# Kernel optimization log

Measured on AMD Instinct MI355X. Metric: run time of the kernel, lower is better.

Reference implementation:

```python
import jax, jax.numpy as jnp
import numpy as np

B, S, D = 4, 2048, 1024

def setup_inputs() -> dict:
    key = jax.random.key(0)
    kx, kq, kk, kv = jax.random.split(key, 4)
    glorot = (6.0 / (D + D)) ** 0.5
    return {
        "x": jax.random.normal(kx, (B, S, D), dtype=jnp.float32),
        "Wq": jax.random.uniform(kq, (D, D), jnp.float32, -glorot, glorot),
        "Wk": jax.random.uniform(kk, (D, D), jnp.float32, -glorot, glorot),
        "Wv": jax.random.uniform(kv, (D, D), jnp.float32, -glorot, glorot),
    }

def reference(x, Wq, Wk, Wv):
    # q,k,v: [B,S,D]
    q = jnp.einsum("bsd,de->bse", x, Wq)
    k = jnp.einsum("bsd,de->bse", x, Wk)
    v = jnp.einsum("bsd,de->bse", x, Wv)
    scale = jnp.sqrt(jnp.asarray(q.shape[-1], q.dtype))
    scores = jnp.einsum("bqd,bkd->bqk", q, k) / scale  # [B,S,S]
    w = jax.nn.softmax(scores, axis=-1)
    return jnp.einsum("bqk,bkd->bqd", w, v)
```

## Files before the change

### kernel.cpp

```cpp
#include <hip/hip_runtime.h>
#include <hip/hip_bf16.h>


typedef _Float16 half_t;
typedef _Float16 half8 __attribute__((ext_vector_type(8)));
typedef _Float16 half4v __attribute__((ext_vector_type(4)));
typedef float f32x4 __attribute__((ext_vector_type(4)));

__device__ __forceinline__ void load16_to_lds(const half_t* g, half_t* l) {
  __builtin_amdgcn_global_load_lds(
      (const __attribute__((address_space(1))) void*)g,
      (__attribute__((address_space(3))) void*)l, 16, 0, 0);
}

#define LGKM0 asm volatile("s_waitcnt lgkmcnt(0)" ::: "memory")
#define LGKM8 asm volatile("s_waitcnt lgkmcnt(8)" ::: "memory")
#define VM0   asm volatile("s_waitcnt vmcnt(0)" ::: "memory")
#define VM4   asm volatile("s_waitcnt vmcnt(4)" ::: "memory")
#define VM6   asm volatile("s_waitcnt vmcnt(6)" ::: "memory")
#define BAR   __builtin_amdgcn_s_barrier()
#define PRIO1 __builtin_amdgcn_s_setprio(1)
#define PRIO0 __builtin_amdgcn_s_setprio(0)

__global__ __launch_bounds__(512, 2) void qkvt_gemm8(
    const half_t* __restrict__ xh, const half_t* __restrict__ wt,
    half_t* __restrict__ qk, half_t* __restrict__ vtg) {
  __shared__ __align__(16) half_t As[2][256 * 64];
  __shared__ __align__(16) half_t Bs[2][256 * 64];

  const int b = blockIdx.x;
  const int x = b & 7, j = b >> 3;
  const int m0 = (x * 4 + (j & 3)) * 256;
  const int n0 = (j >> 2) * 256;

  const int t     = threadIdx.x;
  const int lane  = t & 63;
  const int wave  = t >> 6;
  const int wr128 = (wave >> 2) * 128;
  const int wc64  = (wave & 3) * 64;
  const int lm    = lane & 15;
  const int lq    = lane >> 4;
  const int pos0  = (lq ^ (lm & 7)) * 8;
  const int pos1  = ((4 + lq) ^ (lm & 7)) * 8;
  const int t8    = t * 8;

  const int trow = t >> 3;
  const int tchk = (t & 7) ^ (trow & 7);
  const half_t* gA0 = xh + (size_t)(m0 + trow) * 1024 + tchk * 8;
  const half_t* gB0 = wt + (size_t)(n0 + trow) * 1024 + tchk * 8;

  f32x4 acc[8][4] = {};
  half8 va[4][2], vb0[2][2], vb1[2][2];

#define ST_A(buf, h, kt) do {                                                  \
    load16_to_lds(gA0 + (size_t)((h)*128) * 1024 + (size_t)(kt) * 64,          \
                  &As[buf][(h)*128*64] + t8);                                  \
    load16_to_lds(gA0 + (size_t)((h)*128+64) * 1024 + (size_t)(kt) * 64,       \
                  &As[buf][((h)*128+64)*64] + t8);                             \
  } while (0)
#define ST_B(buf, h, kt) do {                                                  \
    load16_to_lds(gB0 + (size_t)((h)*128) * 1024 + (size_t)(kt) * 64,          \
                  &Bs[buf][(h)*128*64] + t8);                                  \
    load16_to_lds(gB0 + (size_t)((h)*128+64) * 1024 + (size_t)(kt) * 64,       \
                  &Bs[buf][((h)*128+64)*64] + t8);                             \
  } while (0)
#define RD_A(buf, mh) do {                                                     \
    _Pragma("unroll") for (int m = 0; m < 4; ++m) {                            \
      const int ar = wr128 + (mh)*64 + m * 16 + lm;                            \
      va[m][0] = *(const half8*)&As[buf][ar * 64 + pos0];                      \
      va[m][1] = *(const half8*)&As[buf][ar * 64 + pos1];                      \
    } } while (0)
#define RD_B(buf, nh, vb) do {                                                 \
    _Pragma("unroll") for (int n = 0; n < 2; ++n) {                            \
      const int br = wc64 + (nh)*32 + n * 16 + lm;                             \
      vb[n][0] = *(const half8*)&Bs[buf][br * 64 + pos0];                      \
      vb[n][1] = *(const half8*)&Bs[buf][br * 64 + pos1];                      \
    } } while (0)
#define MF_Q(mh, nh, vb) do {                                                  \
    _Pragma("unroll") for (int kk = 0; kk < 2; ++kk)                           \
    _Pragma("unroll") for (int m = 0; m < 4; ++m)                              \
    _Pragma("unroll") for (int n = 0; n < 2; ++n)                              \
      acc[(mh)*4+m][(nh)*2+n] = __builtin_amdgcn_mfma_f32_16x16x32_f16(        \
          va[m][kk], vb[n][kk], acc[(mh)*4+m][(nh)*2+n], 0, 0, 0);             \
  } while (0)

  ST_A(0, 0, 0); ST_A(0, 1, 0);
  ST_B(0, 0, 0); ST_B(0, 1, 0);
  ST_B(1, 0, 1); ST_B(1, 1, 1);
  VM4;
  BAR;

#pragma unroll 1
  for (int i = 0; i < 8; ++i) {
    const int st1 = (2 * i + 1 < 15) ? 2 * i + 1 : 15;
    const int st2 = (2 * i + 2 < 15) ? 2 * i + 2 : 15;
    const int st3 = (2 * i + 3 < 15) ? 2 * i + 3 : 15;
    RD_A(0, 0); RD_B(0, 0, vb0);
    ST_A(1, 0, st1);
    LGKM8;
    BAR; LGKM0;
    PRIO1; MF_Q(0, 0, vb0); PRIO0;
    BAR;
    RD_B(0, 1, vb1);
    ST_A(1, 1, st1);
    BAR; LGKM0;
    PRIO1; MF_Q(0, 1, vb1); PRIO0;
    BAR;
    RD_A(0, 1);
    ST_B(0, 0, st2);
    BAR; LGKM0;
    PRIO1; MF_Q(1, 0, vb0); PRIO0;
    BAR;
    ST_B(0, 1, st2);
    BAR; LGKM0;
    PRIO1; MF_Q(1, 1, vb1); PRIO0;
    VM4;
    BAR;
    RD_A(1, 0); RD_B(1, 0, vb0);
    ST_A(0, 0, st2);
    LGKM8;
    BAR; LGKM0;
    PRIO1; MF_Q(0, 0, vb0); PRIO0;
    BAR;
    RD_B(1, 1, vb1);
    ST_A(0, 1, st2);
    BAR; LGKM0;
    PRIO1; MF_Q(0, 1, vb1); PRIO0;
    BAR;
    RD_A(1, 1);
    ST_B(1, 0, st3);
    BAR; LGKM0;
    PRIO1; MF_Q(1, 0, vb0); PRIO0;
    BAR;
    ST_B(1, 1, st3);
    BAR; LGKM0;
    PRIO1; MF_Q(1, 1, vb1); PRIO0;
    VM4;
    BAR;
  }

#pragma unroll
  for (int m = 0; m < 8; ++m)
#pragma unroll
    for (int n = 0; n < 4; ++n) {
      const int col = n0 + wc64 + n * 16 + lm;
#pragma unroll
      for (int r = 0; r < 4; ++r) {
        const int row = m0 + wr128 + m * 16 + lq * 4 + r;
        qk[(size_t)row * 2048 + col] = (half_t)acc[m][n][r];
      }
    }
#undef ST_A
#undef ST_B
#undef RD_A
#undef RD_B
#undef MF_Q

  const int m0v = (j >> 2) * 128;
  const int n0v = (x * 4 + (j & 3)) * 256;
  const int wmv = (wave >> 2) * 64;
  const int wnv = (wave & 3) * 64;

  const half_t* gA2 = wt + (size_t)2 * 1024 * 1024 +
                      (size_t)(m0v + trow) * 1024 + tchk * 8;
  const half_t* gB2 = xh + (size_t)(n0v + trow) * 1024 + tchk * 8;

  f32x4 acc2[4][4] = {};

#define ST_A2(buf, kt) do {                                                    \
    load16_to_lds(gA2 + (size_t)(kt) * 64, &As[buf][0] + t8);                  \
    load16_to_lds(gA2 + (size_t)64 * 1024 + (size_t)(kt) * 64,                 \
                  &As[buf][64*64] + t8);                                       \
  } while (0)
#define ST_B2(buf, h, kt) do {                                                 \
    load16_to_lds(gB2 + (size_t)((h)*128) * 1024 + (size_t)(kt) * 64,          \
                  &Bs[buf][(h)*128*64] + t8);                                  \
    load16_to_lds(gB2 + (size_t)((h)*128+64) * 1024 + (size_t)(kt) * 64,       \
                  &Bs[buf][((h)*128+64)*64] + t8);                             \
  } while (0)
#define RD_A2(buf, mh) do {                                                    \
    _Pragma("unroll") for (int m = 0; m < 2; ++m) {                            \
      const int ar = wmv + (mh)*32 + m * 16 + lm;                              \
      va[(mh)*2+m][0] = *(const half8*)&As[buf][ar * 64 + pos0];               \
      va[(mh)*2+m][1] = *(const half8*)&As[buf][ar * 64 + pos1];               \
    } } while (0)
#define RD_B2(buf, nh, vb) do {                                                \
    _Pragma("unroll") for (int n = 0; n < 2; ++n) {                            \
      const int br = wnv + (nh)*32 + n * 16 + lm;                              \
      vb[n][0] = *(const half8*)&Bs[buf][br * 64 + pos0];                      \
      vb[n][1] = *(const half8*)&Bs[buf][br * 64 + pos1];                      \
    } } while (0)
#define MF_V(mh, nh, vb) do {                                                  \
    _Pragma("unroll") for (int kk = 0; kk < 2; ++kk)                           \
    _Pragma("unroll") for (int m = 0; m < 2; ++m)                              \
    _Pragma("unroll") for (int n = 0; n < 2; ++n)                              \
      acc2[(mh)*2+m][(nh)*2+n] = __builtin_amdgcn_mfma_f32_16x16x32_f16(       \
          va[(mh)*2+m][kk], vb[n][kk], acc2[(mh)*2+m][(nh)*2+n], 0, 0, 0);     \
  } while (0)

  VM0;
  ST_B2(0, 0, 0); ST_B2(0, 1, 0); ST_A2(0, 0);
  ST_B2(1, 0, 1); ST_B2(1, 1, 1); ST_A2(1, 1);
  VM6;
  BAR;

#pragma unroll 1
  for (int i = 0; i < 8; ++i) {
    const int t2 = (2 * i + 2 < 15) ? 2 * i + 2 : 15;
    const int t3 = (2 * i + 3 < 15) ? 2 * i + 3 : 15;
    RD_A2(0, 0); RD_B2(0, 0, vb0);
    BAR; LGKM0;
    PRIO1; MF_V(0, 0, vb0); PRIO0;
    BAR;
    RD_B2(0, 1, vb1);
    BAR; LGKM0;
    PRIO1; MF_V(0, 1, vb1); PRIO0;
    BAR;
    RD_A2(0, 1);
    ST_B2(0, 0, t2);
    BAR; LGKM0;
    PRIO1; MF_V(1, 0, vb0); PRIO0;
    BAR;
    ST_B2(0, 1, t2); ST_A2(0, t2);
    BAR; LGKM0;
    PRIO1; MF_V(1, 1, vb1); PRIO0;
    VM6;
    BAR;
    RD_A2(1, 0); RD_B2(1, 0, vb0);
    BAR; LGKM0;
    PRIO1; MF_V(0, 0, vb0); PRIO0;
    BAR;
    RD_B2(1, 1, vb1);
    BAR; LGKM0;
    PRIO1; MF_V(0, 1, vb1); PRIO0;
    BAR;
    RD_A2(1, 1);
    ST_B2(1, 0, t3);
    BAR; LGKM0;
    PRIO1; MF_V(1, 0, vb0); PRIO0;
    BAR;
    ST_B2(1, 1, t3); ST_A2(1, t3);
    BAR; LGKM0;
    PRIO1; MF_V(1, 1, vb1); PRIO0;
    VM6;
    BAR;
  }

#pragma unroll
  for (int m = 0; m < 4; ++m)
#pragma unroll
    for (int n = 0; n < 4; ++n) {
      const int col = n0v + wnv + n * 16 + lm;
#pragma unroll
      for (int r = 0; r < 4; ++r) {
        const int row = m0v + wmv + m * 16 + lq * 4 + r;
        vtg[(size_t)row * 8192 + col] = (half_t)acc2[m][n][r];
      }
    }
#undef ST_A2
#undef ST_B2
#undef RD_A2
#undef RD_B2
#undef MF_V
}

__global__ __launch_bounds__(512, 2) void scores_gemm8(
    const half_t* __restrict__ qk, half_t* __restrict__ sc,
    float* __restrict__ lpart) {
  __shared__ __align__(16) half_t As[2][256 * 64];
  __shared__ __align__(16) half_t Bs[2][256 * 64];

  const int id  = blockIdx.x;
  const int x   = id & 7, j = id >> 3;
  const int bx  = j & 7;
  const int z   = x >> 1;
  const int by  = (x & 1) * 4 + (j >> 3);
  const int m0  = by * 256;
  const int n0  = bx * 256;
  const half_t* A  = qk + (size_t)z * 2048 * 2048;
  const half_t* Bm = A + 1024;
  half_t* C = sc + (size_t)z * 2048 * 2048;

  const int t     = threadIdx.x;
  const int lane  = t & 63;
  const int wave  = t >> 6;
  const int wr128 = (wave >> 2) * 128;
  const int wc64  = (wave & 3) * 64;
  const int lm    = lane & 15;
  const int lq    = lane >> 4;
  const int pos0  = (lq ^ (lm & 7)) * 8;
  const int pos1  = ((4 + lq) ^ (lm & 7)) * 8;
  const int t8    = t * 8;

  const int trow = t >> 3;
  const int tchk = (t & 7) ^ (trow & 7);
  const half_t* gA0 = A  + (size_t)(m0 + trow) * 2048 + tchk * 8;
  const half_t* gB0 = Bm + (size_t)(n0 + trow) * 2048 + tchk * 8;

  f32x4 acc[8][4] = {};
  half8 va[4][2], vb0[2][2], vb1[2][2];

#define ST_A(buf, h, kt) do {                                                  \
    load16_to_lds(gA0 + (size_t)((h)*128) * 2048 + (size_t)(kt) * 64,          \
                  &As[buf][(h)*128*64] + t8);                                  \
    load16_to_lds(gA0 + (size_t)((h)*128+64) * 2048 + (size_t)(kt) * 64,       \
                  &As[buf][((h)*128+64)*64] + t8);                             \
  } while (0)
#define ST_B(buf, h, kt) do {                                                  \
    load16_to_lds(gB0 + (size_t)((h)*128) * 2048 + (size_t)(kt) * 64,          \
                  &Bs[buf][(h)*128*64] + t8);                                  \
    load16_to_lds(gB0 + (size_t)((h)*128+64) * 2048 + (size_t)(kt) * 64,       \
                  &Bs[buf][((h)*128+64)*64] + t8);                             \
  } while (0)
#define RD_A(buf, mh) do {                                                     \
    _Pragma("unroll") for (int m = 0; m < 4; ++m) {                            \
      const int ar = wr128 + (mh)*64 + m * 16 + lm;                            \
      va[m][0] = *(const half8*)&As[buf][ar * 64 + pos0];                      \
      va[m][1] = *(const half8*)&As[buf][ar * 64 + pos1];                      \
    } } while (0)
#define RD_B(buf, nh, vb) do {                                                 \
    _Pragma("unroll") for (int n = 0; n < 2; ++n) {                            \
      const int br = wc64 + (nh)*32 + n * 16 + lm;                             \
      vb[n][0] = *(const half8*)&Bs[buf][br * 64 + pos0];                      \
      vb[n][1] = *(const half8*)&Bs[buf][br * 64 + pos1];                      \
    } } while (0)
#define MF_Q(mh, nh, vb) do {                                                  \
    _Pragma("unroll") for (int kk = 0; kk < 2; ++kk)                           \
    _Pragma("unroll") for (int m = 0; m < 4; ++m)                              \
    _Pragma("unroll") for (int n = 0; n < 2; ++n)                              \
      acc[(mh)*4+m][(nh)*2+n] = __builtin_amdgcn_mfma_f32_16x16x32_f16(        \
          va[m][kk], vb[n][kk], acc[(mh)*4+m][(nh)*2+n], 0, 0, 0);             \
  } while (0)

  ST_A(0, 0, 0); ST_A(0, 1, 0);
  ST_B(0, 0, 0); ST_B(0, 1, 0);
  ST_B(1, 0, 1); ST_B(1, 1, 1);
  VM4;
  BAR;

#pragma unroll 1
  for (int i = 0; i < 8; ++i) {
    const int st1 = (2 * i + 1 < 15) ? 2 * i + 1 : 15;
    const int st2 = (2 * i + 2 < 15) ? 2 * i + 2 : 15;
    const int st3 = (2 * i + 3 < 15) ? 2 * i + 3 : 15;
    RD_A(0, 0); RD_B(0, 0, vb0);
    ST_A(1, 0, st1);
    LGKM8;
    BAR; LGKM0;
    PRIO1; MF_Q(0, 0, vb0); PRIO0;
    BAR;
    RD_B(0, 1, vb1);
    ST_A(1, 1, st1);
    BAR; LGKM0;
    PRIO1; MF_Q(0, 1, vb1); PRIO0;
    BAR;
    RD_A(0, 1);
    ST_B(0, 0, st2);
    BAR; LGKM0;
    PRIO1; MF_Q(1, 0, vb0); PRIO0;
    BAR;
    ST_B(0, 1, st2);
    BAR; LGKM0;
    PRIO1; MF_Q(1, 1, vb1); PRIO0;
    VM4;
    BAR;
    RD_A(1, 0); RD_B(1, 0, vb0);
    ST_A(0, 0, st2);
    LGKM8;
    BAR; LGKM0;
    PRIO1; MF_Q(0, 0, vb0); PRIO0;
    BAR;
    RD_B(1, 1, vb1);
    ST_A(0, 1, st2);
    BAR; LGKM0;
    PRIO1; MF_Q(0, 1, vb1); PRIO0;
    BAR;
    RD_A(1, 1);
    ST_B(1, 0, st3);
    BAR; LGKM0;
    PRIO1; MF_Q(1, 0, vb0); PRIO0;
    BAR;
    ST_B(1, 1, st3);
    BAR; LGKM0;
    PRIO1; MF_Q(1, 1, vb1); PRIO0;
    VM4;
    BAR;
  }

  const float scale = 1.0f / 32.0f;
#pragma unroll
  for (int m = 0; m < 8; ++m)
#pragma unroll
    for (int r = 0; r < 4; ++r) {
      const int row = m0 + wr128 + m * 16 + lq * 4 + r;
      float s = 0.f;
#pragma unroll
      for (int n = 0; n < 4; ++n) {
        const int col = n0 + wc64 + n * 16 + lm;
        float v = __expf(acc[m][n][r] * scale - 8.0f);
        s += v;
        C[(size_t)row * 2048 + col] = (half_t)v;
      }
      s += __shfl_xor(s, 1); s += __shfl_xor(s, 2);
      s += __shfl_xor(s, 4); s += __shfl_xor(s, 8);
      if (lm == 0)
        lpart[((size_t)z * 2048 + row) * 32 + bx * 4 + (wave & 3)] = s;
    }
#undef ST_A
#undef ST_B
#undef RD_A
#undef RD_B
#undef MF_Q
}

__global__ __launch_bounds__(512, 2) void pv_gemm8(
    const half_t* __restrict__ sc, const half_t* __restrict__ vtg,
    float* __restrict__ out, const float* __restrict__ lpart) {
  __shared__ __align__(16) half_t As[2][128 * 64];
  __shared__ __align__(16) half_t Bs[2][256 * 64];
  __shared__ float linv[128];

  const int id = blockIdx.x;
  const int x  = id & 7, j = id >> 3;
  const int z  = x >> 1;
  const int m0 = ((x & 1) * 8 + (j >> 2)) * 128;
  const int n0 = (j & 3) * 256;
  const half_t* A  = sc  + (size_t)z * 2048 * 2048;
  const half_t* Bm = vtg + (size_t)z * 2048;
  float* C = out + (size_t)z * 2048 * 1024;

  const int t    = threadIdx.x;
  const int lane = t & 63;
  const int wave = t >> 6;
  const int wmv  = (wave >> 2) * 64;
  const int wnv  = (wave & 3) * 64;
  const int lm   = lane & 15;
  const int lq   = lane >> 4;
  const int pos0 = (lq ^ (lm & 7)) * 8;
  const int pos1 = ((4 + lq) ^ (lm & 7)) * 8;
  const int t8   = t * 8;

  if (t < 128) {
    const float4* lp = (const float4*)&lpart[((size_t)z * 2048 + m0 + t) * 32];
    float s = 0.f;
#pragma unroll
    for (int p = 0; p < 8; ++p) {
      float4 v = lp[p];
      s += v.x + v.y + v.z + v.w;
    }
    linv[t] = 1.0f / s;
  }

  const int trow = t >> 3;
  const int tchk = (t & 7) ^ (trow & 7);
  const half_t* gA2 = A  + (size_t)(m0 + trow) * 2048 + tchk * 8;
  const half_t* gB2 = Bm + (size_t)(n0 + trow) * 8192 + tchk * 8;

  f32x4 acc2[4][4] = {};
  half8 va[4][2], vb0[2][2], vb1[2][2];

#define ST_A2(buf, kt) do {                                                    \
    load16_to_lds(gA2 + (size_t)(kt) * 64, &As[buf][0] + t8);                  \
    load16_to_lds(gA2 + (size_t)64 * 2048 + (size_t)(kt) * 64,                 \
                  &As[buf][64*64] + t8);                                       \
  } while (0)
#define ST_B2(buf, h, kt) do {                                                 \
    load16_to_lds(gB2 + (size_t)((h)*128) * 8192 + (size_t)(kt) * 64,          \
                  &Bs[buf][(h)*128*64] + t8);                                  \
    load16_to_lds(gB2 + (size_t)((h)*128+64) * 8192 + (size_t)(kt) * 64,       \
                  &Bs[buf][((h)*128+64)*64] + t8);                             \
  } while (0)
#define RD_A2(buf, mh) do {                                                    \
    _Pragma("unroll") for (int m = 0; m < 2; ++m) {                            \
      const int ar = wmv + (mh)*32 + m * 16 + lm;                              \
      va[(mh)*2+m][0] = *(const half8*)&As[buf][ar * 64 + pos0];               \
      va[(mh)*2+m][1] = *(const half8*)&As[buf][ar * 64 + pos1];               \
    } } while (0)
#define RD_B2(buf, nh, vb) do {                                                \
    _Pragma("unroll") for (int n = 0; n < 2; ++n) {                            \
      const int br = wnv + (nh)*32 + n * 16 + lm;                              \
      vb[n][0] = *(const half8*)&Bs[buf][br * 64 + pos0];                      \
      vb[n][1] = *(const half8*)&Bs[buf][br * 64 + pos1];                      \
    } } while (0)
#define MF_V(mh, nh, vb) do {                                                  \
    _Pragma("unroll") for (int kk = 0; kk < 2; ++kk)                           \
    _Pragma("unroll") for (int m = 0; m < 2; ++m)                              \
    _Pragma("unroll") for (int n = 0; n < 2; ++n)                              \
      acc2[(mh)*2+m][(nh)*2+n] = __builtin_amdgcn_mfma_f32_16x16x32_f16(       \
          va[(mh)*2+m][kk], vb[n][kk], acc2[(mh)*2+m][(nh)*2+n], 0, 0, 0);     \
  } while (0)

  ST_B2(0, 0, 0); ST_B2(0, 1, 0); ST_A2(0, 0);
  ST_B2(1, 0, 1); ST_B2(1, 1, 1); ST_A2(1, 1);
  VM6;
  BAR;

#pragma unroll 1
  for (int i = 0; i < 16; ++i) {
    const int t2 = (2 * i + 2 < 31) ? 2 * i + 2 : 31;
    const int t3 = (2 * i + 3 < 31) ? 2 * i + 3 : 31;
    RD_A2(0, 0); RD_B2(0, 0, vb0);
    BAR; LGKM0;
    PRIO1; MF_V(0, 0, vb0); PRIO0;
    BAR;
    RD_B2(0, 1, vb1);
    BAR; LGKM0;
    PRIO1; MF_V(0, 1, vb1); PRIO0;
    BAR;
    RD_A2(0, 1);
    ST_B2(0, 0, t2);
    BAR; LGKM0;
    PRIO1; MF_V(1, 0, vb0); PRIO0;
    BAR;
    ST_B2(0, 1, t2); ST_A2(0, t2);
    BAR; LGKM0;
    PRIO1; MF_V(1, 1, vb1); PRIO0;
    VM6;
    BAR;
    RD_A2(1, 0); RD_B2(1, 0, vb0);
    BAR; LGKM0;
    PRIO1; MF_V(0, 0, vb0); PRIO0;
    BAR;
    RD_B2(1, 1, vb1);
    BAR; LGKM0;
    PRIO1; MF_V(0, 1, vb1); PRIO0;
    BAR;
    RD_A2(1, 1);
    ST_B2(1, 0, t3);
    BAR; LGKM0;
    PRIO1; MF_V(1, 0, vb0); PRIO0;
    BAR;
    ST_B2(1, 1, t3); ST_A2(1, t3);
    BAR; LGKM0;
    PRIO1; MF_V(1, 1, vb1); PRIO0;
    VM6;
    BAR;
  }

#pragma unroll
  for (int m = 0; m < 4; ++m)
#pragma unroll
    for (int r = 0; r < 4; ++r) {
      const int lrow = wmv + m * 16 + lq * 4 + r;
      const float inv = linv[lrow];
      const int row = m0 + lrow;
#pragma unroll
      for (int n = 0; n < 4; ++n) {
        const int col = n0 + wnv + n * 16 + lm;
        C[(size_t)row * 1024 + col] = acc2[m][n][r] * inv;
      }
    }
#undef ST_A2
#undef ST_B2
#undef RD_A2
#undef RD_B2
#undef MF_V
}

__global__ __launch_bounds__(256) void prep(
    const float* __restrict__ x, half_t* __restrict__ xh,
    const float* __restrict__ Wq, const float* __restrict__ Wk,
    const float* __restrict__ Wv, half_t* __restrict__ wt) {
  __shared__ half_t tile[32][33];
  const int b = blockIdx.x;
  const int t = threadIdx.x;
  if (b < 8192) {
    const int i = (b * 256 + t) * 4;
    const float4 v = *reinterpret_cast<const float4*>(x + i);
    half4v o;
    o.x = (half_t)v.x; o.y = (half_t)v.y; o.z = (half_t)v.z; o.w = (half_t)v.w;
    *reinterpret_cast<half4v*>(xh + i) = o;
  } else {
    int bb = b - 8192;
    const int w = bb >> 10; bb &= 1023;
    const float* in = (w == 0) ? Wq : (w == 1) ? Wk : Wv;
    half_t* o = wt + (size_t)w * 1024 * 1024;
    const int r0 = (bb >> 5) * 32, c0 = (bb & 31) * 32;
    const int tx = t & 31, ty = t >> 5;
#pragma unroll
    for (int i = 0; i < 32; i += 8)
      tile[ty + i][tx] = (half_t)in[(size_t)(r0 + ty + i) * 1024 + c0 + tx];
    __syncthreads();
#pragma unroll
    for (int i = 0; i < 32; i += 8)
      o[(size_t)(c0 + ty + i) * 1024 + r0 + tx] = tile[tx][ty + i];
  }
}

extern "C" void kernel_launch(void* const* d_in, const int* in_sizes, int n_in,
                              void* d_out, int out_size, void* d_ws, size_t ws_size,
                              hipStream_t stream) {
  constexpr int Bb = 4, S = 2048, D = 1024;
  constexpr size_t MS = (size_t)Bb * S;

  const float* x  = (const float*)d_in[0];
  const float* Wq = (const float*)d_in[1];
  const float* Wk = (const float*)d_in[2];
  const float* Wv = (const float*)d_in[3];
  float* out = (float*)d_out;

  char* p = (char*)d_ws;
  half_t* xh    = (half_t*)p; p += MS * D * 2;
  half_t* wt    = (half_t*)p; p += (size_t)3 * D * D * 2;
  half_t* qk    = (half_t*)p; p += MS * (size_t)(2 * D) * 2;
  half_t* vtg   = (half_t*)p; p += (size_t)D * MS * 2;
  half_t* sc    = (half_t*)p; p += (size_t)Bb * S * S * 2;
  float*  lpart = (float*)p;  p += MS * 32 * 4;

  prep<<<11264, 256, 0, stream>>>(x, xh, Wq, Wk, Wv, wt);
  qkvt_gemm8<<<256, 512, 0, stream>>>(xh, wt, qk, vtg);
  scores_gemm8<<<256, 512, 0, stream>>>(qk, sc, lpart);
  pv_gemm8<<<256, 512, 0, stream>>>(sc, vtg, out, lpart);
}
```

Before: 220.7 us.

## Fuse prep and three GEMM kernels into one cooperative persistent kernel

Merges the fp16 conversion/transpose prep kernel, the QKV projection GEMM, the scores GEMM and the PV GEMM into a single cooperative kernel of 256 blocks, with grid-wide syncs between phases. The prep work is redistributed across the 256 blocks, and the weight-transpose tiles reuse the GEMM's shared-memory buffers. This removes three kernel launches and their inter-kernel gaps. In exchange it adds grid-barrier cost and ties the grid size to full co-residency. It also enlarges the shared footprint, because the PV phase now shares 256-row A buffers.

```diff
diff --git a/kernel.cpp b/kernel.cpp
--- a/kernel.cpp
+++ b/kernel.cpp
@@ -1,5 +1,8 @@
 #include <hip/hip_runtime.h>
 #include <hip/hip_bf16.h>
+#include <hip/hip_cooperative_groups.h>
+
+namespace cg = cooperative_groups;
 
 
 typedef _Float16 half_t;
@@ -22,35 +25,78 @@
 #define PRIO1 __builtin_amdgcn_s_setprio(1)
 #define PRIO0 __builtin_amdgcn_s_setprio(0)
 
-__global__ __launch_bounds__(512, 2) void qkvt_gemm8(
-    const half_t* __restrict__ xh, const half_t* __restrict__ wt,
-    half_t* __restrict__ qk, half_t* __restrict__ vtg) {
+__global__ __launch_bounds__(512, 2) void fused_attn(
+    const float* __restrict__ x, const float* __restrict__ Wq,
+    const float* __restrict__ Wk, const float* __restrict__ Wv,
+    half_t* __restrict__ xh, half_t* __restrict__ wt,
+    half_t* __restrict__ qk, half_t* __restrict__ vtg,
+    half_t* __restrict__ sc, float* __restrict__ lpart,
+    float* __restrict__ out) {
   __shared__ __align__(16) half_t As[2][256 * 64];
   __shared__ __align__(16) half_t Bs[2][256 * 64];
-
-  const int b = blockIdx.x;
-  const int x = b & 7, j = b >> 3;
-  const int m0 = (x * 4 + (j & 3)) * 256;
-  const int n0 = (j >> 2) * 256;
-
-  const int t     = threadIdx.x;
-  const int lane  = t & 63;
-  const int wave  = t >> 6;
+  __shared__ float linv[128];
+
+  cg::grid_group gg = cg::this_grid();
+
+  const int t    = threadIdx.x;
+  const int lane = t & 63;
+  const int wave = t >> 6;
+  const int lm   = lane & 15;
+  const int lq   = lane >> 4;
+  const int pos0 = (lq ^ (lm & 7)) * 8;
+  const int pos1 = ((4 + lq) ^ (lm & 7)) * 8;
+  const int t8   = t * 8;
+  const int trow = t >> 3;
+  const int tchk = (t & 7) ^ (trow & 7);
   const int wr128 = (wave >> 2) * 128;
   const int wc64  = (wave & 3) * 64;
-  const int lm    = lane & 15;
-  const int lq    = lane >> 4;
-  const int pos0  = (lq ^ (lm & 7)) * 8;
-  const int pos1  = ((4 + lq) ^ (lm & 7)) * 8;
-  const int t8    = t * 8;
-
-  const int trow = t >> 3;
-  const int tchk = (t & 7) ^ (trow & 7);
-  const half_t* gA0 = xh + (size_t)(m0 + trow) * 1024 + tchk * 8;
-  const half_t* gB0 = wt + (size_t)(n0 + trow) * 1024 + tchk * 8;
-
-  f32x4 acc[8][4] = {};
-  half8 va[4][2], vb0[2][2], vb1[2][2];
+
+  {
+    const int gtid = blockIdx.x * 512 + t;
+#pragma unroll
+    for (int k = 0; k < 16; ++k) {
+      const size_t i = ((size_t)gtid + (size_t)k * 131072) * 4;
+      const float4 v = *reinterpret_cast<const float4*>(x + i);
+      half4v o;
+      o.x = (half_t)v.x; o.y = (half_t)v.y; o.z = (half_t)v.z; o.w = (half_t)v.w;
+      *reinterpret_cast<half4v*>(xh + i) = o;
+    }
+    half_t (*tp)[32][33] = reinterpret_cast<half_t (*)[32][33]>(&As[0][0]);
+    const int sub = t >> 8;
+    const int tt  = t & 255;
+    const int tx = tt & 31, ty = tt >> 5;
+    for (int it = 0; it < 6; ++it) {
+      const int tile = blockIdx.x * 12 + it * 2 + sub;
+      const int w    = tile >> 10;
+      const int rem  = tile & 1023;
+      const float* in = (w == 0) ? Wq : (w == 1) ? Wk : Wv;
+      half_t* o = wt + (size_t)w * 1024 * 1024;
+      const int r0 = (rem >> 5) * 32, c0 = (rem & 31) * 32;
+      __syncthreads();
+#pragma unroll
+      for (int i2 = 0; i2 < 32; i2 += 8)
+        tp[sub][ty + i2][tx] =
+            (half_t)in[(size_t)(r0 + ty + i2) * 1024 + c0 + tx];
+      __syncthreads();
+#pragma unroll
+      for (int i2 = 0; i2 < 32; i2 += 8)
+        o[(size_t)(c0 + ty + i2) * 1024 + r0 + tx] = tp[sub][tx][ty + i2];
+    }
+    VM0;
+  }
+  gg.sync();
+
+  {
+    const int b = blockIdx.x;
+    const int xc = b & 7, j = b >> 3;
+    const int m0 = (xc * 4 + (j & 3)) * 256;
+    const int n0 = (j >> 2) * 256;
+
+    const half_t* gA0 = xh + (size_t)(m0 + trow) * 1024 + tchk * 8;
+    const half_t* gB0 = wt + (size_t)(n0 + trow) * 1024 + tchk * 8;
+
+    f32x4 acc[8][4] = {};
+    half8 va[4][2], vb0[2][2], vb1[2][2];
 
 #define ST_A(buf, h, kt) do {                                                  \
     load16_to_lds(gA0 + (size_t)((h)*128) * 1024 + (size_t)(kt) * 64,          \
@@ -84,88 +130,88 @@
           va[m][kk], vb[n][kk], acc[(mh)*4+m][(nh)*2+n], 0, 0, 0);             \
   } while (0)
 
-  ST_A(0, 0, 0); ST_A(0, 1, 0);
-  ST_B(0, 0, 0); ST_B(0, 1, 0);
-  ST_B(1, 0, 1); ST_B(1, 1, 1);
-  VM4;
-  BAR;
-
-#pragma unroll 1
-  for (int i = 0; i < 8; ++i) {
-    const int st1 = (2 * i + 1 < 15) ? 2 * i + 1 : 15;
-    const int st2 = (2 * i + 2 < 15) ? 2 * i + 2 : 15;
-    const int st3 = (2 * i + 3 < 15) ? 2 * i + 3 : 15;
-    RD_A(0, 0); RD_B(0, 0, vb0);
-    ST_A(1, 0, st1);
-    LGKM8;
-    BAR; LGKM0;
-    PRIO1; MF_Q(0, 0, vb0); PRIO0;
-    BAR;
-    RD_B(0, 1, vb1);
-    ST_A(1, 1, st1);
-    BAR; LGKM0;
-    PRIO1; MF_Q(0, 1, vb1); PRIO0;
-    BAR;
-    RD_A(0, 1);
-    ST_B(0, 0, st2);
-    BAR; LGKM0;
-    PRIO1; MF_Q(1, 0, vb0); PRIO0;
-    BAR;
-    ST_B(0, 1, st2);
-    BAR; LGKM0;
-    PRIO1; MF_Q(1, 1, vb1); PRIO0;
+    ST_A(0, 0, 0); ST_A(0, 1, 0);
+    ST_B(0, 0, 0); ST_B(0, 1, 0);
+    ST_B(1, 0, 1); ST_B(1, 1, 1);
     VM4;
     BAR;
-    RD_A(1, 0); RD_B(1, 0, vb0);
-    ST_A(0, 0, st2);
-    LGKM8;
-    BAR; LGKM0;
-    PRIO1; MF_Q(0, 0, vb0); PRIO0;
-    BAR;
-    RD_B(1, 1, vb1);
-    ST_A(0, 1, st2);
-    BAR; LGKM0;
-    PRIO1; MF_Q(0, 1, vb1); PRIO0;
-    BAR;
-    RD_A(1, 1);
-    ST_B(1, 0, st3);
-    BAR; LGKM0;
-    PRIO1; MF_Q(1, 0, vb0); PRIO0;
-    BAR;
-    ST_B(1, 1, st3);
-    BAR; LGKM0;
-    PRIO1; MF_Q(1, 1, vb1); PRIO0;
-    VM4;
-    BAR;
-  }
-
-#pragma unroll
-  for (int m = 0; m < 8; ++m)
-#pragma unroll
-    for (int n = 0; n < 4; ++n) {
-      const int col = n0 + wc64 + n * 16 + lm;
-#pragma unroll
-      for (int r = 0; r < 4; ++r) {
-        const int row = m0 + wr128 + m * 16 + lq * 4 + r;
-        qk[(size_t)row * 2048 + col] = (half_t)acc[m][n][r];
+
+#pragma unroll 1
+    for (int i = 0; i < 8; ++i) {
+      const int st1 = (2 * i + 1 < 15) ? 2 * i + 1 : 15;
+      const int st2 = (2 * i + 2 < 15) ? 2 * i + 2 : 15;
+      const int st3 = (2 * i + 3 < 15) ? 2 * i + 3 : 15;
+      RD_A(0, 0); RD_B(0, 0, vb0);
+      ST_A(1, 0, st1);
+      LGKM8;
+      BAR; LGKM0;
+      PRIO1; MF_Q(0, 0, vb0); PRIO0;
+      BAR;
+      RD_B(0, 1, vb1);
+      ST_A(1, 1, st1);
+      BAR; LGKM0;
+      PRIO1; MF_Q(0, 1, vb1); PRIO0;
+      BAR;
+      RD_A(0, 1);
+      ST_B(0, 0, st2);
+      BAR; LGKM0;
+      PRIO1; MF_Q(1, 0, vb0); PRIO0;
+      BAR;
+      ST_B(0, 1, st2);
+      BAR; LGKM0;
+      PRIO1; MF_Q(1, 1, vb1); PRIO0;
+      VM4;
+      BAR;
+      RD_A(1, 0); RD_B(1, 0, vb0);
+      ST_A(0, 0, st2);
+      LGKM8;
+      BAR; LGKM0;
+      PRIO1; MF_Q(0, 0, vb0); PRIO0;
+      BAR;
+      RD_B(1, 1, vb1);
+      ST_A(0, 1, st2);
+      BAR; LGKM0;
+      PRIO1; MF_Q(0, 1, vb1); PRIO0;
+      BAR;
+      RD_A(1, 1);
+      ST_B(1, 0, st3);
+      BAR; LGKM0;
+      PRIO1; MF_Q(1, 0, vb0); PRIO0;
+      BAR;
+      ST_B(1, 1, st3);
+      BAR; LGKM0;
+      PRIO1; MF_Q(1, 1, vb1); PRIO0;
+      VM4;
+      BAR;
+    }
+
+#pragma unroll
+    for (int m = 0; m < 8; ++m)
+#pragma unroll
+      for (int n = 0; n < 4; ++n) {
+        const int col = n0 + wc64 + n * 16 + lm;
+#pragma unroll
+        for (int r = 0; r < 4; ++r) {
+          const int row = m0 + wr128 + m * 16 + lq * 4 + r;
+          qk[(size_t)row * 2048 + col] = (half_t)acc[m][n][r];
+        }
       }
-    }
 #undef ST_A
 #undef ST_B
 #undef RD_A
 #undef RD_B
 #undef MF_Q
 
-  const int m0v = (j >> 2) * 128;
-  const int n0v = (x * 4 + (j & 3)) * 256;
-  const int wmv = (wave >> 2) * 64;
-  const int wnv = (wave & 3) * 64;
-
-  const half_t* gA2 = wt + (size_t)2 * 1024 * 1024 +
-                      (size_t)(m0v + trow) * 1024 + tchk * 8;
-  const half_t* gB2 = xh + (size_t)(n0v + trow) * 1024 + tchk * 8;
-
-  f32x4 acc2[4][4] = {};
+    const int m0v = (j >> 2) * 128;
+    const int n0v = (xc * 4 + (j & 3)) * 256;
+    const int wmv = (wave >> 2) * 64;
+    const int wnv = (wave & 3) * 64;
+
+    const half_t* gA2 = wt + (size_t)2 * 1024 * 1024 +
+                        (size_t)(m0v + trow) * 1024 + tchk * 8;
+    const half_t* gB2 = xh + (size_t)(n0v + trow) * 1024 + tchk * 8;
+
+    f32x4 acc2[4][4] = {};
 
 #define ST_A2(buf, kt) do {                                                    \
     load16_to_lds(gA2 + (size_t)(kt) * 64, &As[buf][0] + t8);                  \
@@ -198,107 +244,91 @@
           va[(mh)*2+m][kk], vb[n][kk], acc2[(mh)*2+m][(nh)*2+n], 0, 0, 0);     \
   } while (0)
 
-  VM0;
-  ST_B2(0, 0, 0); ST_B2(0, 1, 0); ST_A2(0, 0);
-  ST_B2(1, 0, 1); ST_B2(1, 1, 1); ST_A2(1, 1);
-  VM6;
-  BAR;
-
-#pragma unroll 1
-  for (int i = 0; i < 8; ++i) {
-    const int t2 = (2 * i + 2 < 15) ? 2 * i + 2 : 15;
-    const int t3 = (2 * i + 3 < 15) ? 2 * i + 3 : 15;
-    RD_A2(0, 0); RD_B2(0, 0, vb0);
-    BAR; LGKM0;
-    PRIO1; MF_V(0, 0, vb0); PRIO0;
-    BAR;
-    RD_B2(0, 1, vb1);
-    BAR; LGKM0;
-    PRIO1; MF_V(0, 1, vb1); PRIO0;
-    BAR;
-    RD_A2(0, 1);
-    ST_B2(0, 0, t2);
-    BAR; LGKM0;
-    PRIO1; MF_V(1, 0, vb0); PRIO0;
-    BAR;
-    ST_B2(0, 1, t2); ST_A2(0, t2);
-    BAR; LGKM0;
-    PRIO1; MF_V(1, 1, vb1); PRIO0;
+    VM0;
+    ST_B2(0, 0, 0); ST_B2(0, 1, 0); ST_A2(0, 0);
+    ST_B2(1, 0, 1); ST_B2(1, 1, 1); ST_A2(1, 1);
     VM6;
     BAR;
-    RD_A2(1, 0); RD_B2(1, 0, vb0);
-    BAR; LGKM0;
-    PRIO1; MF_V(0, 0, vb0); PRIO0;
-    BAR;
-    RD_B2(1, 1, vb1);
-    BAR; LGKM0;
-    PRIO1; MF_V(0, 1, vb1); PRIO0;
-    BAR;
-    RD_A2(1, 1);
-    ST_B2(1, 0, t3);
-    BAR; LGKM0;
-    PRIO1; MF_V(1, 0, vb0); PRIO0;
-    BAR;
-    ST_B2(1, 1, t3); ST_A2(1, t3);
-    BAR; LGKM0;
-    PRIO1; MF_V(1, 1, vb1); PRIO0;
-    VM6;
-    BAR;
-  }
-
-#pragma unroll
-  for (int m = 0; m < 4; ++m)
-#pragma unroll
-    for (int n = 0; n < 4; ++n) {
-      const int col = n0v + wnv + n * 16 + lm;
-#pragma unroll
-      for (int r = 0; r < 4; ++r) {
-        const int row = m0v + wmv + m * 16 + lq * 4 + r;
-        vtg[(size_t)row * 8192 + col] = (half_t)acc2[m][n][r];
+
+#pragma unroll 1
+    for (int i = 0; i < 8; ++i) {
+      const int t2 = (2 * i + 2 < 15) ? 2 * i + 2 : 15;
+      const int t3 = (2 * i + 3 < 15) ? 2 * i + 3 : 15;
+      RD_A2(0, 0); RD_B2(0, 0, vb0);
+      BAR; LGKM0;
+      PRIO1; MF_V(0, 0, vb0); PRIO0;
+      BAR;
+      RD_B2(0, 1, vb1);
+      BAR; LGKM0;
+      PRIO1; MF_V(0, 1, vb1); PRIO0;
+      BAR;
+      RD_A2(0, 1);
+      ST_B2(0, 0, t2);
+      BAR; LGKM0;
+      PRIO1; MF_V(1, 0, vb0); PRIO0;
+      BAR;
+      ST_B2(0, 1, t2); ST_A2(0, t2);
+      BAR; LGKM0;
+      PRIO1; MF_V(1, 1, vb1); PRIO0;
+      VM6;
+      BAR;
+      RD_A2(1, 0); RD_B2(1, 0, vb0);
+      BAR; LGKM0;
+      PRIO1; MF_V(0, 0, vb0); PRIO0;
+      BAR;
+      RD_B2(1, 1, vb1);
+      BAR; LGKM0;
+      PRIO1; MF_V(0, 1, vb1); PRIO0;
+      BAR;
+      RD_A2(1, 1);
+      ST_B2(1, 0, t3);
+      BAR; LGKM0;
+      PRIO1; MF_V(1, 0, vb0); PRIO0;
+      BAR;
+      ST_B2(1, 1, t3); ST_A2(1, t3);
+      BAR; LGKM0;
+      PRIO1; MF_V(1, 1, vb1); PRIO0;
+      VM6;
+      BAR;
+    }
+
+#pragma unroll
+    for (int m = 0; m < 4; ++m)
+#pragma unroll
+      for (int n = 0; n < 4; ++n) {
+        const int col = n0v + wnv + n * 16 + lm;
+#pragma unroll
+        for (int r = 0; r < 4; ++r) {
+          const int row = m0v + wmv + m * 16 + lq * 4 + r;
+          vtg[(size_t)row * 8192 + col] = (half_t)acc2[m][n][r];
+        }
       }
-    }
 #undef ST_A2
 #undef ST_B2
 #undef RD_A2
 #undef RD_B2
 #undef MF_V
-}
-
-__global__ __launch_bounds__(512, 2) void scores_gemm8(
-    const half_t* __restrict__ qk, half_t* __restrict__ sc,
-    float* __restrict__ lpart) {
-  __shared__ __align__(16) half_t As[2][256 * 64];
-  __shared__ __align__(16) half_t Bs[2][256 * 64];
-
-  const int id  = blockIdx.x;
-  const int x   = id & 7, j = id >> 3;
-  const int bx  = j & 7;
-  const int z   = x >> 1;
-  const int by  = (x & 1) * 4 + (j >> 3);
-  const int m0  = by * 256;
-  const int n0  = bx * 256;
-  const half_t* A  = qk + (size_t)z * 2048 * 2048;
-  const half_t* Bm = A + 1024;
-  half_t* C = sc + (size_t)z * 2048 * 2048;
-
-  const int t     = threadIdx.x;
-  const int lane  = t & 63;
-  const int wave  = t >> 6;
-  const int wr128 = (wave >> 2) * 128;
-  const int wc64  = (wave & 3) * 64;
-  const int lm    = lane & 15;
-  const int lq    = lane >> 4;
-  const int pos0  = (lq ^ (lm & 7)) * 8;
-  const int pos1  = ((4 + lq) ^ (lm & 7)) * 8;
-  const int t8    = t * 8;
-
-  const int trow = t >> 3;
-  const int tchk = (t & 7) ^ (trow & 7);
-  const half_t* gA0 = A  + (size_t)(m0 + trow) * 2048 + tchk * 8;
-  const half_t* gB0 = Bm + (size_t)(n0 + trow) * 2048 + tchk * 8;
-
-  f32x4 acc[8][4] = {};
-  half8 va[4][2], vb0[2][2], vb1[2][2];
+    VM0;
+  }
+  gg.sync();
+
+  {
+    const int id = blockIdx.x;
+    const int xc = id & 7, j = id >> 3;
+    const int bx = j & 7;
+    const int z  = xc >> 1;
+    const int by = (xc & 1) * 4 + (j >> 3);
+    const int m0 = by * 256;
+    const int n0 = bx * 256;
+    const half_t* A  = qk + (size_t)z * 2048 * 2048;
+    const half_t* Bm = A + 1024;
+    half_t* C = sc + (size_t)z * 2048 * 2048;
+
+    const half_t* gA0 = A  + (size_t)(m0 + trow) * 2048 + tchk * 8;
+    const half_t* gB0 = Bm + (size_t)(n0 + trow) * 2048 + tchk * 8;
+
+    f32x4 acc[8][4] = {};
+    half8 va[4][2], vb0[2][2], vb1[2][2];
 
 #define ST_A(buf, h, kt) do {                                                  \
     load16_to_lds(gA0 + (size_t)((h)*128) * 2048 + (size_t)(kt) * 64,          \
@@ -332,132 +362,119 @@
           va[m][kk], vb[n][kk], acc[(mh)*4+m][(nh)*2+n], 0, 0, 0);             \
   } while (0)
 
-  ST_A(0, 0, 0); ST_A(0, 1, 0);
-  ST_B(0, 0, 0); ST_B(0, 1, 0);
-  ST_B(1, 0, 1); ST_B(1, 1, 1);
-  VM4;
-  BAR;
-
-#pragma unroll 1
-  for (int i = 0; i < 8; ++i) {
-    const int st1 = (2 * i + 1 < 15) ? 2 * i + 1 : 15;
-    const int st2 = (2 * i + 2 < 15) ? 2 * i + 2 : 15;
-    const int st3 = (2 * i + 3 < 15) ? 2 * i + 3 : 15;
-    RD_A(0, 0); RD_B(0, 0, vb0);
-    ST_A(1, 0, st1);
-    LGKM8;
-    BAR; LGKM0;
-    PRIO1; MF_Q(0, 0, vb0); PRIO0;
-    BAR;
-    RD_B(0, 1, vb1);
-    ST_A(1, 1, st1);
-    BAR; LGKM0;
-    PRIO1; MF_Q(0, 1, vb1); PRIO0;
-    BAR;
-    RD_A(0, 1);
-    ST_B(0, 0, st2);
-    BAR; LGKM0;
-    PRIO1; MF_Q(1, 0, vb0); PRIO0;
-    BAR;
-    ST_B(0, 1, st2);
-    BAR; LGKM0;
-    PRIO1; MF_Q(1, 1, vb1); PRIO0;
+    ST_A(0, 0, 0); ST_A(0, 1, 0);
+    ST_B(0, 0, 0); ST_B(0, 1, 0);
+    ST_B(1, 0, 1); ST_B(1, 1, 1);
     VM4;
     BAR;
-    RD_A(1, 0); RD_B(1, 0, vb0);
-    ST_A(0, 0, st2);
-    LGKM8;
-    BAR; LGKM0;
-    PRIO1; MF_Q(0, 0, vb0); PRIO0;
-    BAR;
-    RD_B(1, 1, vb1);
-    ST_A(0, 1, st2);
-    BAR; LGKM0;
-    PRIO1; MF_Q(0, 1, vb1); PRIO0;
-    BAR;
-    RD_A(1, 1);
-    ST_B(1, 0, st3);
-    BAR; LGKM0;
-    PRIO1; MF_Q(1, 0, vb0); PRIO0;
-    BAR;
-    ST_B(1, 1, st3);
-    BAR; LGKM0;
-    PRIO1; MF_Q(1, 1, vb1); PRIO0;
-    VM4;
-    BAR;
-  }
-
-  const float scale = 1.0f / 32.0f;
-#pragma unroll
-  for (int m = 0; m < 8; ++m)
-#pragma unroll
-    for (int r = 0; r < 4; ++r) {
-      const int row = m0 + wr128 + m * 16 + lq * 4 + r;
-      float s = 0.f;
-#pragma unroll
-      for (int n = 0; n < 4; ++n) {
-        const int col = n0 + wc64 + n * 16 + lm;
-        float v = __expf(acc[m][n][r] * scale - 8.0f);
-        s += v;
-        C[(size_t)row * 2048 + col] = (half_t)v;
+
+#pragma unroll 1
+    for (int i = 0; i < 8; ++i) {
+      const int st1 = (2 * i + 1 < 15) ? 2 * i + 1 : 15;
+      const int st2 = (2 * i + 2 < 15) ? 2 * i + 2 : 15;
+      const int st3 = (2 * i + 3 < 15) ? 2 * i + 3 : 15;
+      RD_A(0, 0); RD_B(0, 0, vb0);
+      ST_A(1, 0, st1);
+      LGKM8;
+      BAR; LGKM0;
+      PRIO1; MF_Q(0, 0, vb0); PRIO0;
+      BAR;
+      RD_B(0, 1, vb1);
+      ST_A(1, 1, st1);
+      BAR; LGKM0;
+      PRIO1; MF_Q(0, 1, vb1); PRIO0;
+      BAR;
+      RD_A(0, 1);
+      ST_B(0, 0, st2);
+      BAR; LGKM0;
+      PRIO1; MF_Q(1, 0, vb0); PRIO0;
+      BAR;
+      ST_B(0, 1, st2);
+      BAR; LGKM0;
+      PRIO1; MF_Q(1, 1, vb1); PRIO0;
+      VM4;
+      BAR;
+      RD_A(1, 0); RD_B(1, 0, vb0);
+      ST_A(0, 0, st2);
+      LGKM8;
+      BAR; LGKM0;
+      PRIO1; MF_Q(0, 0, vb0); PRIO0;
+      BAR;
+      RD_B(1, 1, vb1);
+      ST_A(0, 1, st2);
+      BAR; LGKM0;
+      PRIO1; MF_Q(0, 1, vb1); PRIO0;
+      BAR;
+      RD_A(1, 1);
+      ST_B(1, 0, st3);
+      BAR; LGKM0;
+      PRIO1; MF_Q(1, 0, vb0); PRIO0;
+      BAR;
+      ST_B(1, 1, st3);
+      BAR; LGKM0;
+      PRIO1; MF_Q(1, 1, vb1); PRIO0;
+      VM4;
+      BAR;
+    }
+
+    const float scale = 1.0f / 32.0f;
+#pragma unroll
+    for (int m = 0; m < 8; ++m)
+#pragma unroll
+      for (int r = 0; r < 4; ++r) {
+        const int row = m0 + wr128 + m * 16 + lq * 4 + r;
+        float s = 0.f;
+#pragma unroll
+        for (int n = 0; n < 4; ++n) {
+          const int col = n0 + wc64 + n * 16 + lm;
+          float v = __expf(acc[m][n][r] * scale - 8.0f);
+          s += v;
+          C[(size_t)row * 2048 + col] = (half_t)v;
+        }
+        s += __shfl_xor(s, 1); s += __shfl_xor(s, 2);
+        s += __shfl_xor(s, 4); s += __shfl_xor(s, 8);
+        if (lm == 0)
+          lpart[((size_t)z * 2048 + row) * 32 + bx * 4 + (wave & 3)] = s;
       }
-      s += __shfl_xor(s, 1); s += __shfl_xor(s, 2);
-      s += __shfl_xor(s, 4); s += __shfl_xor(s, 8);
-      if (lm == 0)
-        lpart[((size_t)z * 2048 + row) * 32 + bx * 4 + (wave & 3)] = s;
-    }
 #undef ST_A
 #undef ST_B
 #undef RD_A
 #undef RD_B
 #undef MF_Q
-}
-
-__global__ __launch_bounds__(512, 2) void pv_gemm8(
-    const half_t* __restrict__ sc, const half_t* __restrict__ vtg,
-    float* __restrict__ out, const float* __restrict__ lpart) {
-  __shared__ __align__(16) half_t As[2][128 * 64];
-  __shared__ __align__(16) half_t Bs[2][256 * 64];
-  __shared__ float linv[128];
-
-  const int id = blockIdx.x;
-  const int x  = id & 7, j = id >> 3;
-  const int z  = x >> 1;
-  const int m0 = ((x & 1) * 8 + (j >> 2)) * 128;
-  const int n0 = (j & 3) * 256;
-  const half_t* A  = sc  + (size_t)z * 2048 * 2048;
-  const half_t* Bm = vtg + (size_t)z * 2048;
-  float* C = out + (size_t)z * 2048 * 1024;
-
-  const int t    = threadIdx.x;
-  const int lane = t & 63;
-  const int wave = t >> 6;
-  const int wmv  = (wave >> 2) * 64;
-  const int wnv  = (wave & 3) * 64;
-  const int lm   = lane & 15;
-  const int lq   = lane >> 4;
-  const int pos0 = (lq ^ (lm & 7)) * 8;
-  const int pos1 = ((4 + lq) ^ (lm & 7)) * 8;
-  const int t8   = t * 8;
-
-  if (t < 128) {
-    const float4* lp = (const float4*)&lpart[((size_t)z * 2048 + m0 + t) * 32];
-    float s = 0.f;
-#pragma unroll
-    for (int p = 0; p < 8; ++p) {
-      float4 v = lp[p];
-      s += v.x + v.y + v.z + v.w;
+    VM0;
+  }
+  gg.sync();
+
+  {
+    const int id = blockIdx.x;
+    const int xc = id & 7, j = id >> 3;
+    const int z  = xc >> 1;
+    const int m0 = ((xc & 1) * 8 + (j >> 2)) * 128;
+    const int n0 = (j & 3) * 256;
+    const half_t* A  = sc  + (size_t)z * 2048 * 2048;
+    const half_t* Bm = vtg + (size_t)z * 2048;
+    float* C = out + (size_t)z * 2048 * 1024;
+
+    const int wmv = (wave >> 2) * 64;
+    const int wnv = (wave & 3) * 64;
+
+    if (t < 128) {
+      const float4* lp =
+          (const float4*)&lpart[((size_t)z * 2048 + m0 + t) * 32];
+      float s = 0.f;
+#pragma unroll
+      for (int p = 0; p < 8; ++p) {
+        float4 v = lp[p];
+        s += v.x + v.y + v.z + v.w;
+      }
+      linv[t] = 1.0f / s;
     }
-    linv[t] = 1.0f / s;
-  }
-
-  const int trow = t >> 3;
-  const int tchk = (t & 7) ^ (trow & 7);
-  const half_t* gA2 = A  + (size_t)(m0 + trow) * 2048 + tchk * 8;
-  const half_t* gB2 = Bm + (size_t)(n0 + trow) * 8192 + tchk * 8;
-
-  f32x4 acc2[4][4] = {};
-  half8 va[4][2], vb0[2][2], vb1[2][2];
+
+    const half_t* gA2 = A  + (size_t)(m0 + trow) * 2048 + tchk * 8;
+    const half_t* gB2 = Bm + (size_t)(n0 + trow) * 8192 + tchk * 8;
+
+    f32x4 acc2[4][4] = {};
+    half8 va[4][2], vb0[2][2], vb1[2][2];
 
 #define ST_A2(buf, kt) do {                                                    \
     load16_to_lds(gA2 + (size_t)(kt) * 64, &As[buf][0] + t8);                  \
@@ -490,100 +507,71 @@
           va[(mh)*2+m][kk], vb[n][kk], acc2[(mh)*2+m][(nh)*2+n], 0, 0, 0);     \
   } while (0)
 
-  ST_B2(0, 0, 0); ST_B2(0, 1, 0); ST_A2(0, 0);
-  ST_B2(1, 0, 1); ST_B2(1, 1, 1); ST_A2(1, 1);
-  VM6;
-  BAR;
-
-#pragma unroll 1
-  for (int i = 0; i < 16; ++i) {
-    const int t2 = (2 * i + 2 < 31) ? 2 * i + 2 : 31;
-    const int t3 = (2 * i + 3 < 31) ? 2 * i + 3 : 31;
-    RD_A2(0, 0); RD_B2(0, 0, vb0);
-    BAR; LGKM0;
-    PRIO1; MF_V(0, 0, vb0); PRIO0;
-    BAR;
-    RD_B2(0, 1, vb1);
-    BAR; LGKM0;
-    PRIO1; MF_V(0, 1, vb1); PRIO0;
-    BAR;
-    RD_A2(0, 1);
-    ST_B2(0, 0, t2);
-    BAR; LGKM0;
-    PRIO1; MF_V(1, 0, vb0); PRIO0;
-    BAR;
-    ST_B2(0, 1, t2); ST_A2(0, t2);
-    BAR; LGKM0;
-    PRIO1; MF_V(1, 1, vb1); PRIO0;
+    ST_B2(0, 0, 0); ST_B2(0, 1, 0); ST_A2(0, 0);
+    ST_B2(1, 0, 1); ST_B2(1, 1, 1); ST_A2(1, 1);
     VM6;
     BAR;
-    RD_A2(1, 0); RD_B2(1, 0, vb0);
-    BAR; LGKM0;
-    PRIO1; MF_V(0, 0, vb0); PRIO0;
-    BAR;
-    RD_B2(1, 1, vb1);
-    BAR; LGKM0;
-    PRIO1; MF_V(0, 1, vb1); PRIO0;
-    BAR;
-    RD_A2(1, 1);
-    ST_B2(1, 0, t3);
-    BAR; LGKM0;
-    PRIO1; MF_V(1, 0, vb0); PRIO0;
-    BAR;
-    ST_B2(1, 1, t3); ST_A2(1, t3);
-    BAR; LGKM0;
-    PRIO1; MF_V(1, 1, vb1); PRIO0;
-    VM6;
-    BAR;
-  }
-
-#pragma unroll
-  for (int m = 0; m < 4; ++m)
-#pragma unroll
-    for (int r = 0; r < 4; ++r) {
-      const int lrow = wmv + m * 16 + lq * 4 + r;
-      const float inv = linv[lrow];
-      const int row = m0 + lrow;
-#pragma unroll
-      for (int n = 0; n < 4; ++n) {
-        const int col = n0 + wnv + n * 16 + lm;
-        C[(size_t)row * 1024 + col] = acc2[m][n][r] * inv;
+
+#pragma unroll 1
+    for (int i = 0; i < 16; ++i) {
+      const int t2 = (2 * i + 2 < 31) ? 2 * i + 2 : 31;
+      const int t3 = (2 * i + 3 < 31) ? 2 * i + 3 : 31;
+      RD_A2(0, 0); RD_B2(0, 0, vb0);
+      BAR; LGKM0;
+      PRIO1; MF_V(0, 0, vb0); PRIO0;
+      BAR;
+      RD_B2(0, 1, vb1);
+      BAR; LGKM0;
+      PRIO1; MF_V(0, 1, vb1); PRIO0;
+      BAR;
+      RD_A2(0, 1);
+      ST_B2(0, 0, t2);
+      BAR; LGKM0;
+      PRIO1; MF_V(1, 0, vb0); PRIO0;
+      BAR;
+      ST_B2(0, 1, t2); ST_A2(0, t2);
+      BAR; LGKM0;
+      PRIO1; MF_V(1, 1, vb1); PRIO0;
+      VM6;
+      BAR;
+      RD_A2(1, 0); RD_B2(1, 0, vb0);
+      BAR; LGKM0;
+      PRIO1; MF_V(0, 0, vb0); PRIO0;
+      BAR;
+      RD_B2(1, 1, vb1);
+      BAR; LGKM0;
+      PRIO1; MF_V(0, 1, vb1); PRIO0;
+      BAR;
+      RD_A2(1, 1);
+      ST_B2(1, 0, t3);
+      BAR; LGKM0;
+      PRIO1; MF_V(1, 0, vb0); PRIO0;
+      BAR;
+      ST_B2(1, 1, t3); ST_A2(1, t3);
+      BAR; LGKM0;
+      PRIO1; MF_V(1, 1, vb1); PRIO0;
+      VM6;
+      BAR;
+    }
+
+#pragma unroll
+    for (int m = 0; m < 4; ++m)
+#pragma unroll
+      for (int r = 0; r < 4; ++r) {
+        const int lrow = wmv + m * 16 + lq * 4 + r;
+        const float inv = linv[lrow];
+        const int row = m0 + lrow;
+#pragma unroll
+        for (int n = 0; n < 4; ++n) {
+          const int col = n0 + wnv + n * 16 + lm;
+          C[(size_t)row * 1024 + col] = acc2[m][n][r] * inv;
+        }
       }
-    }
 #undef ST_A2
 #undef ST_B2
 #undef RD_A2
 #undef RD_B2
 #undef MF_V
-}
-
-__global__ __launch_bounds__(256) void prep(
-    const float* __restrict__ x, half_t* __restrict__ xh,
-    const float* __restrict__ Wq, const float* __restrict__ Wk,
-    const float* __restrict__ Wv, half_t* __restrict__ wt) {
-  __shared__ half_t tile[32][33];
-  const int b = blockIdx.x;
-  const int t = threadIdx.x;
-  if (b < 8192) {
-    const int i = (b * 256 + t) * 4;
-    const float4 v = *reinterpret_cast<const float4*>(x + i);
-    half4v o;
-    o.x = (half_t)v.x; o.y = (half_t)v.y; o.z = (half_t)v.z; o.w = (half_t)v.w;
-    *reinterpret_cast<half4v*>(xh + i) = o;
-  } else {
-    int bb = b - 8192;
-    const int w = bb >> 10; bb &= 1023;
-    const float* in = (w == 0) ? Wq : (w == 1) ? Wk : Wv;
-    half_t* o = wt + (size_t)w * 1024 * 1024;
-    const int r0 = (bb >> 5) * 32, c0 = (bb & 31) * 32;
-    const int tx = t & 31, ty = t >> 5;
-#pragma unroll
-    for (int i = 0; i < 32; i += 8)
-      tile[ty + i][tx] = (half_t)in[(size_t)(r0 + ty + i) * 1024 + c0 + tx];
-    __syncthreads();
-#pragma unroll
-    for (int i = 0; i < 32; i += 8)
-      o[(size_t)(c0 + ty + i) * 1024 + r0 + tx] = tile[tx][ty + i];
   }
 }
 
@@ -607,8 +595,9 @@
   half_t* sc    = (half_t*)p; p += (size_t)Bb * S * S * 2;
   float*  lpart = (float*)p;  p += MS * 32 * 4;
 
-  prep<<<11264, 256, 0, stream>>>(x, xh, Wq, Wk, Wv, wt);
-  qkvt_gemm8<<<256, 512, 0, stream>>>(xh, wt, qk, vtg);
-  scores_gemm8<<<256, 512, 0, stream>>>(qk, sc, lpart);
-  pv_gemm8<<<256, 512, 0, stream>>>(sc, vtg, out, lpart);
+  void* args[] = {(void*)&x,  (void*)&Wq, (void*)&Wk,  (void*)&Wv,
+                  (void*)&xh, (void*)&wt, (void*)&qk,  (void*)&vtg,
+                  (void*)&sc, (void*)&lpart, (void*)&out};
+  hipLaunchCooperativeKernel((const void*)fused_attn, dim3(256), dim3(512),
+                             args, 0, stream);
 }
```

Result: slower. 328.9 us (+49.0%).
